# Optimization experiments

Measured on AMD Instinct MI355X. Metric: run time of the kernel, lower is better.

The kernel has to match this reference:

```python
import jax, jax.numpy as jnp
import numpy as np

HIDDEN = 4096       # in_features of gate/up proj
INTER = 11008       # intermediate_size (per projection)
GROUP = 128         # GPTQ group size
B, S = 4, 2048
NIB = jnp.uint32(0xF)


def _pack_rows(nib):
    """Pack 4-bit values along rows: [8*R, C] uint32 -> [R, C] uint32."""
    r = nib.reshape(-1, 8, nib.shape[-1])
    shifts = (jnp.arange(8, dtype=jnp.uint32) * 4)[None, :, None]
    return jnp.sum(r << shifts, axis=1, dtype=jnp.uint32)  # disjoint bits -> sum == OR


def _pack_cols(nib):
    """Pack 4-bit values along cols: [G, 8*C] uint32 -> [G, C] uint32."""
    r = nib.reshape(nib.shape[0], -1, 8)
    shifts = (jnp.arange(8, dtype=jnp.uint32) * 4)[None, None, :]
    return jnp.sum(r << shifts, axis=2, dtype=jnp.uint32)


def setup_inputs() -> dict:
    key = jax.random.key(0)
    ks = jax.random.split(key, 7)
    n_groups = HIDDEN // GROUP          # 32 groups for gate_up
    n_groups_d = INTER // GROUP         # 86 groups for down

    x = jax.random.normal(ks[0], (B, S, HIDDEN), jnp.float32)

    # gate_up_proj: in=HIDDEN, out=2*INTER
    nib_w_gu = jax.random.randint(ks[1], (HIDDEN, 2 * INTER), 0, 16).astype(jnp.uint32)
    nib_z_gu = jax.random.randint(ks[2], (n_groups, 2 * INTER), 0, 15).astype(jnp.uint32)
    qweight_gu = _pack_rows(nib_w_gu)                          # [HIDDEN//8, 2*INTER]
    qzeros_gu = _pack_cols(nib_z_gu)                           # [n_groups, 2*INTER//8]
    scales_gu = jax.random.uniform(ks[3], (n_groups, 2 * INTER), jnp.float32, 0.005, 0.02)
    g_idx_gu = (jnp.arange(HIDDEN, dtype=jnp.int32) // GROUP)

    # down_proj: in=INTER, out=HIDDEN
    nib_w_d = jax.random.randint(ks[4], (INTER, HIDDEN), 0, 16).astype(jnp.uint32)
    nib_z_d = jax.random.randint(ks[5], (n_groups_d, HIDDEN), 0, 15).astype(jnp.uint32)
    qweight_down = _pack_rows(nib_w_d)                         # [INTER//8, HIDDEN]
    qzeros_down = _pack_cols(nib_z_d)                          # [n_groups_d, HIDDEN//8]
    scales_down = jax.random.uniform(ks[6], (n_groups_d, HIDDEN), jnp.float32, 0.005, 0.02)
    g_idx_down = (jnp.arange(INTER, dtype=jnp.int32) // GROUP)

    return {
        "x": x,
        "qweight_gu": qweight_gu, "qzeros_gu": qzeros_gu,
        "scales_gu": scales_gu, "g_idx_gu": g_idx_gu,
        "qweight_down": qweight_down, "qzeros_down": qzeros_down,
        "scales_down": scales_down, "g_idx_down": g_idx_down,
    }


def _dequant(qw, qz, sc, g_idx):
    """GPTQ v2 dequant: W[i,j] = sc[g[i],j] * (wq[i,j] - (zq[g[i],j] + 1))."""
    shifts = jnp.arange(8, dtype=jnp.uint32) * 4
    # unpack qweight along rows: [R, C] -> [8*R, C]
    wq = ((qw[:, None, :] >> shifts[None, :, None]) & NIB)
    wq = wq.reshape(-1, qw.shape[1]).astype(jnp.float32)
    # unpack qzeros along cols: [G, C//8] -> [G, C]; +1 per GPTQ v2 convention
    zq = ((qz[:, :, None] >> shifts[None, None, :]) & NIB)
    zq = zq.reshape(qz.shape[0], -1).astype(jnp.float32) + 1.0
    return sc[g_idx] * (wq - zq[g_idx])  # [in, out]


def reference(x, qweight_gu, qzeros_gu, scales_gu, g_idx_gu,
              qweight_down, qzeros_down, scales_down, g_idx_down):
    w_gu = _dequant(qweight_gu, qzeros_gu, scales_gu, g_idx_gu)          # [HIDDEN, 2*INTER]
    inter = jnp.einsum('bsh,hf->bsf', x, w_gu)                            # [B,S,2*INTER]
    gate, up = inter[..., :INTER], inter[..., INTER:]
    h = jax.nn.silu(gate) * up                                            # SwiGLU
    w_d = _dequant(qweight_down, qzeros_down, scales_down, g_idx_down)   # [INTER, HIDDEN]
    return jnp.einsum('bsf,fh->bsh', h, w_d)
```

## Files before the change

### kernel.cpp

```cpp
#include <hip/hip_runtime.h>
#include <stdint.h>

#define HIDDEN 4096
#define INTER  11008
#define NTOK   8192
#define WROW   22016

typedef __bf16 bf16;
typedef __bf16 bf16x8 __attribute__((ext_vector_type(8)));
typedef _Float16 f16;
typedef _Float16 f16x2 __attribute__((ext_vector_type(2)));
typedef _Float16 f16x8 __attribute__((ext_vector_type(8)));
typedef float  f32x4  __attribute__((ext_vector_type(4)));

__device__ __forceinline__ void gload16(const void* g, void* l) {
  __builtin_amdgcn_global_load_lds(
      (const __attribute__((address_space(1))) void*)g,
      (__attribute__((address_space(3))) void*)l, 16, 0, 0);
}
__device__ __forceinline__ void gload4(const void* g, void* l) {
  __builtin_amdgcn_global_load_lds(
      (const __attribute__((address_space(1))) void*)g,
      (__attribute__((address_space(3))) void*)l, 4, 0, 0);
}

__global__ __launch_bounds__(256) void cvt_f16_kernel(const float* __restrict__ x,
                                                      f16* __restrict__ y) {
  const int i = (blockIdx.x * 256 + threadIdx.x) * 8;
  f32x4 a = *(const f32x4*)(x + i);
  f32x4 b = *(const f32x4*)(x + i + 4);
  f16x8 v;
#pragma unroll
  for (int j = 0; j < 4; ++j) { v[2 * j] = (f16)a[j]; v[2 * j + 1] = (f16)b[j]; }
  *(f16x8*)(y + i) = v;
}

__global__ __launch_bounds__(256) void spak_kernel(const uint32_t* __restrict__ qz,
                                                   const float* __restrict__ sc,
                                                   uint32_t* __restrict__ outp) {
  const int idx = blockIdx.x * 256 + threadIdx.x;
  const int gq = idx / WROW;
  const int n = idx - gq * WROW;
  const int grp = n >> 5, win = n & 31;
  const int jg = (win < 16) ? grp * 16 + win : INTER + grp * 16 + (win - 16);
  const float s = sc[(size_t)gq * WROW + jg];
  const uint32_t z = (qz[(size_t)gq * (WROW / 8) + (jg >> 3)] >> ((jg & 7) * 4)) & 15u;
  union { f16 h[2]; uint32_t u; } a, b;
  a.h[0] = (f16)s; a.h[1] = (f16)s;
  b.h[0] = (f16)(float)(1025u + z); b.h[1] = b.h[0];
  outp[(size_t)idx * 2 + 0] = a.u;
  outp[(size_t)idx * 2 + 1] = b.u;
}

__global__ __launch_bounds__(256) void dequant_kernel(const uint32_t* __restrict__ qw,
                                                      const uint32_t* __restrict__ qz,
                                                      const float* __restrict__ sc,
                                                      bf16* __restrict__ out,
                                                      int J, int Kout) {
  __shared__ __align__(16) bf16 T[64 * 256];
  const int tid = threadIdx.x;
  const int tx = tid & 63, ty = tid >> 6;
  const int j0 = blockIdx.x * 64, r0 = blockIdx.y * 32;
  const int j = j0 + tx;
  const int J8 = J >> 3;
#pragma unroll
  for (int i = 0; i < 8; ++i) {
    const int r = r0 + ty * 8 + i;
    const int g = r >> 4;
    const uint32_t w = qw[(size_t)r * J + j];
    const float s = sc[(size_t)g * J + j];
    const uint32_t zb = (qz[(size_t)g * J8 + (j >> 3)] >> ((j & 7) * 4)) & 15u;
    const float zoff = (float)(zb + 1u);
    bf16x8 v;
#pragma unroll
    for (int e = 0; e < 8; ++e) {
      const float wv = (float)((w >> (e * 4)) & 15u);
      v[e] = (bf16)(s * (wv - zoff));
    }
    const int lb = (tx * 512 + (ty * 8 + i) * 16) ^ ((tx & 31) << 4);
    *(bf16x8*)((char*)T + lb) = v;
  }
  __syncthreads();
#pragma unroll
  for (int u = 0; u < 8; ++u) {
    const int unit = u * 256 + tid;
    const int jj = unit >> 5;
    const int ob = (unit & 31) * 16;
    const int lb = (jj * 512 + ob) ^ ((jj & 31) << 4);
    bf16x8 v = *(const bf16x8*)((const char*)T + lb);
    *(bf16x8*)(out + (size_t)(j0 + jj) * Kout + r0 * 8 + (ob >> 1)) = v;
  }
}

#define OFF_BP 65536
#define OFF_SPK 82176

#define BAR __builtin_amdgcn_s_barrier()
#define LGKM0                                              \
  do {                                                     \
    asm volatile("s_waitcnt lgkmcnt(0)" ::: "memory");     \
    __builtin_amdgcn_sched_barrier(0);                     \
  } while (0)
#define VM2 asm volatile("s_waitcnt vmcnt(2)" ::: "memory")
#define VM3 asm volatile("s_waitcnt vmcnt(3)" ::: "memory")

#define STG_A(buf, h, tt)                                                      \
  do {                                                                         \
    gload16(sA00 + ((size_t)((h) * 128) * (HIDDEN * 2)) + (size_t)(tt) * 128,  \
            lds + (buf) * 32768 + (h) * 16384 + w * 1024);                     \
    gload16(sA00 + ((size_t)((h) * 128 + 64) * (HIDDEN * 2)) + (size_t)(tt) * 128, \
            lds + (buf) * 32768 + (h) * 16384 + 8192 + w * 1024);              \
  } while (0)

#define STG_B(buf, tt)                                                        \
  gload16(bsrc + (size_t)(8 * (tt) + w) * WROW,                               \
          lds + OFF_BP + (buf) * 8320 + w * 1040)

#define STG_SPK(gt)                                                           \
  gload4(spakg + ((size_t)(gt) * WROW + n0) * 2 + tid,                        \
         lds + OFF_SPK + ((gt) & 3) * 2048 + w * 256)

__device__ __forceinline__ f16x8 unpack8s(uint32_t u, f16x2 s2, f16x2 k2) {
  const uint32_t MSK = 0x000F000Fu, M = 0x64006400u;
  uint32_t q0 = (u & MSK) | M;
  uint32_t q1 = ((u >> 4) & MSK) | M;
  uint32_t q2 = ((u >> 8) & MSK) | M;
  uint32_t q3 = ((u >> 12) & MSK) | M;
  f16x2 w0 = (__builtin_bit_cast(f16x2, q0) - k2) * s2;
  f16x2 w1 = (__builtin_bit_cast(f16x2, q1) - k2) * s2;
  f16x2 w2 = (__builtin_bit_cast(f16x2, q2) - k2) * s2;
  f16x2 w3 = (__builtin_bit_cast(f16x2, q3) - k2) * s2;
  f16x8 r;
  r[0] = w0[0]; r[1] = w0[1]; r[2] = w1[0]; r[3] = w1[1];
  r[4] = w2[0]; r[5] = w2[1]; r[6] = w3[0]; r[7] = w3[1];
  return r;
}

#define UNP_SL(AVH, BUIDX, NH, NJ, KK, R, C)                                   \
  do {                                                                         \
    bv[NJ][KK] = unpack8s(bu[BUIDX], s2r[NH][NJ], k2r[NH][NJ]);                \
    _Pragma("unroll") for (int mi = 0; mi < 4; ++mi)                           \
      acc[(R) + mi][C] = __builtin_amdgcn_mfma_f32_16x16x32_f16(               \
          AVH[mi][KK], bv[NJ][KK], acc[(R) + mi][C], 0, 0, 0);                 \
  } while (0)

#define MFMA16(AVH, R, CBASE)                                                  \
  do {                                                                         \
    _Pragma("unroll") for (int kk = 0; kk < 2; ++kk)                           \
      _Pragma("unroll") for (int nj = 0; nj < 2; ++nj)                         \
        _Pragma("unroll") for (int mi = 0; mi < 4; ++mi)                       \
          acc[(R) + mi][(CBASE) + nj] = __builtin_amdgcn_mfma_f32_16x16x32_f16(\
              AVH[mi][kk], bv[nj][kk], acc[(R) + mi][(CBASE) + nj], 0, 0, 0);  \
  } while (0)

__global__ __launch_bounds__(512, 2) void gemm1q(const f16* __restrict__ A,
                                                 const uint32_t* __restrict__ qw,
                                                 const uint32_t* __restrict__ spakg,
                                                 bf16* __restrict__ H) {
  extern __shared__ char lds[];
  const int tid = threadIdx.x;
  const int lane = tid & 63, w = tid >> 6;
  const int wr = w >> 2, wc = w & 3;
  const int fr = lane & 15, fg = lane >> 4;
  constexpr int NT = HIDDEN / 64;

  const int wg = blockIdx.x;
  const int nb = wg % (WROW / 256), mb = wg / (WROW / 256);
  const int m0 = mb << 8, n0 = nb << 8;

  const int rbase = tid >> 3;
  const int cbyte0 = (tid & 7) * 16;
  const int cL0 = cbyte0 ^ ((rbase & 7) << 4);
  const char* sA00 = (const char*)A + (size_t)(m0 + rbase) * (size_t)(HIDDEN * 2) + cL0;

  const int n4 = n0 + lane * 4;
  const int grp4 = n4 >> 5, win4 = n4 & 31;
  const int jg4 = (win4 < 16) ? grp4 * 16 + win4 : INTER + grp4 * 16 + (win4 - 16);
  const uint32_t* bsrc = qw + jg4;

  const int swz = (fr & 7) << 4;
  const int ck[2] = {(fg * 16) ^ swz, (64 + fg * 16) ^ swz};
  const int aro = (wr * 64 + fr) * 128;
  auto lda = [&](int buf, int mh, int mi, int kk) -> f16x8 {
    return *(const f16x8*)(lds + buf * 32768 + mh * 16384 + aro + mi * 2048 + ck[kk]);
  };
  const int ncol[2][2] = {{wc * 32 + fr, wc * 32 + 16 + fr},
                          {wc * 32 + 128 + fr, wc * 32 + 144 + fr}};

  f32x4 acc[8][4];
#pragma unroll
  for (int i = 0; i < 8; ++i)
#pragma unroll
    for (int j = 0; j < 4; ++j) acc[i][j] = (f32x4)0.0f;
  f16x8 av0[4][2], av1[4][2], bv[2][2];
  uint32_t bu[8];
  f16x2 s2r[2][2], k2r[2][2];

  STG_SPK(0);
  STG_A(0, 0, 0);
  STG_B(0, 0);
  STG_A(0, 1, 0);
  VM2;
  BAR;

  for (int t = 0; t < NT; ++t) {
    const int cb = t & 1, nx = cb ^ 1, g = t >> 1;
    const int t1 = (t + 1 < NT) ? t + 1 : 0;

#pragma unroll
    for (int mi = 0; mi < 4; ++mi) { av0[mi][0] = lda(cb, 0, mi, 0); av0[mi][1] = lda(cb, 0, mi, 1); }
#pragma unroll
    for (int nh = 0; nh < 2; ++nh)
#pragma unroll
      for (int nj = 0; nj < 2; ++nj)
#pragma unroll
        for (int kk = 0; kk < 2; ++kk)
          bu[nh * 4 + nj * 2 + kk] = *(const uint32_t*)(
              lds + OFF_BP + cb * 8320 + (kk * 4 + fg) * 1040 + ncol[nh][nj] * 4);
    if ((t & 1) == 0) {
      const char* sp = lds + OFF_SPK + (g & 3) * 2048;
#pragma unroll
      for (int nh = 0; nh < 2; ++nh)
#pragma unroll
        for (int nj = 0; nj < 2; ++nj) {
          s2r[nh][nj] = *(const f16x2*)(sp + ncol[nh][nj] * 8);
          k2r[nh][nj] = *(const f16x2*)(sp + ncol[nh][nj] * 8 + 4);
        }
    }
    STG_A(nx, 0, t1);
    STG_B(nx, t1);
    VM3;
    BAR; LGKM0;
    __builtin_amdgcn_s_setprio(1);
    UNP_SL(av0, 0, 0, 0, 0, 0, 0);
    UNP_SL(av0, 1, 0, 0, 1, 0, 0);
    UNP_SL(av0, 2, 0, 1, 0, 0, 1);
    UNP_SL(av0, 3, 0, 1, 1, 0, 1);
    __builtin_amdgcn_s_setprio(0);
    __builtin_amdgcn_sched_barrier(0);
    BAR;

#pragma unroll
    for (int mi = 0; mi < 4; ++mi) { av1[mi][0] = lda(cb, 1, mi, 0); av1[mi][1] = lda(cb, 1, mi, 1); }
    if (t & 1) {
      const int gt = (g + 1 < 32) ? g + 1 : 31;
      STG_SPK(gt);
    }
    STG_A(nx, 1, t1);
    BAR; LGKM0;
    __builtin_amdgcn_s_setprio(1);
    MFMA16(av1, 4, 0);
    __builtin_amdgcn_s_setprio(0);
    __builtin_amdgcn_sched_barrier(0);
    BAR;

    __builtin_amdgcn_s_setprio(1);
    UNP_SL(av1, 4, 1, 0, 0, 4, 2);
    UNP_SL(av1, 5, 1, 0, 1, 4, 2);
    UNP_SL(av1, 6, 1, 1, 0, 4, 3);
    UNP_SL(av1, 7, 1, 1, 1, 4, 3);
    MFMA16(av0, 0, 2);
    __builtin_amdgcn_s_setprio(0);
    __builtin_amdgcn_sched_barrier(0);
    VM2;
    BAR;
  }
  asm volatile("s_waitcnt vmcnt(0)" ::: "memory");

#pragma unroll
  for (int mh = 0; mh < 2; ++mh)
#pragma unroll
    for (int mi = 0; mi < 4; ++mi)
#pragma unroll
      for (int nh = 0; nh < 2; ++nh) {
        const f32x4 gv4 = acc[mh * 4 + mi][nh * 2];
        const f32x4 uv4 = acc[mh * 4 + mi][nh * 2 + 1];
        const int col = (n0 >> 1) + wc * 16 + nh * 64 + fr;
#pragma unroll
        for (int rr = 0; rr < 4; ++rr) {
          const int row = m0 + wr * 64 + mh * 128 + mi * 16 + fg * 4 + rr;
          const float gv = gv4[rr], uv = uv4[rr];
          H[(size_t)row * INTER + col] = (bf16)(gv / (1.0f + __expf(-gv)) * uv);
        }
      }
}

#define OFF_A2 0
#define OFF_B2 32768

#define STG2(mat, buf, h, t)                                                   \
  do {                                                                         \
    gload16(s##mat[h][0] + (size_t)(t) * 128,                                  \
            lds + (buf) * 65536 + OFF_##mat + (h) * 16384 + w * 1024);         \
    gload16(s##mat[h][1] + (size_t)(t) * 128,                                  \
            lds + (buf) * 65536 + OFF_##mat + (h) * 16384 + 8192 + w * 1024);  \
  } while (0)
#define VM6 asm volatile("s_waitcnt vmcnt(6)" ::: "memory")

#define MFMA_Q2(MH, NH)                                                        \
  do {                                                                         \
    __builtin_amdgcn_s_setprio(1);                                             \
    _Pragma("unroll") for (int kk = 0; kk < 2; ++kk) {                         \
      _Pragma("unroll") for (int nj = 0; nj < 2; ++nj) {                       \
        _Pragma("unroll") for (int mi = 0; mi < 4; ++mi) {                     \
          acc[(MH)*4 + mi][(NH)*2 + nj] = __builtin_amdgcn_mfma_f32_16x16x32_bf16( \
              av[mi][kk], bv[nj][kk], acc[(MH)*4 + mi][(NH)*2 + nj], 0, 0, 0); \
        }                                                                      \
      }                                                                        \
    }                                                                          \
    __builtin_amdgcn_s_setprio(0);                                             \
    __builtin_amdgcn_sched_barrier(0);                                         \
  } while (0)

template <int K, int NT, int NNB>
__global__ __launch_bounds__(512, 2) void gemm8p(const bf16* __restrict__ A,
                                                 const bf16* __restrict__ Bm,
                                                 float* __restrict__ O) {
  extern __shared__ char lds[];
  const int tid = threadIdx.x;
  const int lane = tid & 63, w = tid >> 6;
  const int wr = w >> 2, wc = w & 3;
  const int fr = lane & 15, fg = lane >> 4;

  const int wg = blockIdx.x;
  const int nb = wg % NNB, mb = wg / NNB;
  const int m0 = mb << 8, n0 = nb << 8;

  const char* sA2[2][2];
  const char* sB2[2][2];
#pragma unroll
  for (int h = 0; h < 2; ++h)
#pragma unroll
    for (int l = 0; l < 2; ++l) {
      const int d = h * 16384 + (l * 512 + tid) * 16;
      const int r = d >> 7;
      const int cL = (d & 127) ^ ((r & 7) << 4);
      sA2[h][l] = (const char*)A + (size_t)(m0 + r) * (size_t)(K * 2) + cL;
      sB2[h][l] = (const char*)Bm + (size_t)(n0 + r) * (size_t)(K * 2) + cL;
    }

  const int swz = (fr & 7) << 4;
  const int ck[2] = {(fg * 16) ^ swz, (64 + fg * 16) ^ swz};
  const int aro = (wr * 64 + fr) * 128;
  const int bro = OFF_B2 + (wc * 32 + fr) * 128;

  auto lda = [&](int buf, int mh, int mi, int kk) -> bf16x8 {
    return *(const bf16x8*)(lds + buf * 65536 + mh * 16384 + aro + mi * 2048 + ck[kk]);
  };
  auto ldb = [&](int buf, int nh, int nj, int kk) -> bf16x8 {
    return *(const bf16x8*)(lds + buf * 65536 + bro + nh * 16384 + nj * 2048 + ck[kk]);
  };

  f32x4 acc[8][4];
#pragma unroll
  for (int i = 0; i < 8; ++i)
#pragma unroll
    for (int j = 0; j < 4; ++j) acc[i][j] = (f32x4)0.0f;
  bf16x8 av[4][2], bv[2][2];

  STG2(A2, 0, 0, 0);
  STG2(B2, 0, 0, 0);
  STG2(B2, 0, 1, 0);
  STG2(A2, 0, 1, 0);
  STG2(A2, 1, 0, 1);
  STG2(B2, 1, 1, 1);
  STG2(A2, 1, 1, 1);
  VM6;
  BAR;

  for (int t = 0; t < NT; ++t) {
    const int cb = t & 1, nx = cb ^ 1;
    const int t1 = (t + 1 < NT) ? t + 1 : 0;
    const int t2 = (t + 2 < NT) ? t + 2 : 0;

#pragma unroll
    for (int mi = 0; mi < 4; ++mi) { av[mi][0] = lda(cb, 0, mi, 0); av[mi][1] = lda(cb, 0, mi, 1); }
#pragma unroll
    for (int nj = 0; nj < 2; ++nj) { bv[nj][0] = ldb(cb, 0, nj, 0); bv[nj][1] = ldb(cb, 0, nj, 1); }
    STG2(B2, nx, 0, t1);
    BAR; LGKM0;
    MFMA_Q2(0, 0);
    BAR;

#pragma unroll
    for (int nj = 0; nj < 2; ++nj) { bv[nj][0] = ldb(cb, 1, nj, 0); bv[nj][1] = ldb(cb, 1, nj, 1); }
    STG2(A2, cb, 0, t2);
    BAR; LGKM0;
    MFMA_Q2(0, 1);
    BAR;

#pragma unroll
    for (int mi = 0; mi < 4; ++mi) { av[mi][0] = lda(cb, 1, mi, 0); av[mi][1] = lda(cb, 1, mi, 1); }
    STG2(B2, cb, 1, t2);
    BAR; LGKM0;
    MFMA_Q2(1, 1);
    BAR;

#pragma unroll
    for (int nj = 0; nj < 2; ++nj) { bv[nj][0] = ldb(cb, 0, nj, 0); bv[nj][1] = ldb(cb, 0, nj, 1); }
    STG2(A2, cb, 1, t2);
    VM6;
    BAR; LGKM0;
    MFMA_Q2(1, 0);
    BAR;
  }

#pragma unroll
  for (int mh = 0; mh < 2; ++mh)
#pragma unroll
    for (int mi = 0; mi < 4; ++mi)
#pragma unroll
      for (int nh = 0; nh < 2; ++nh)
#pragma unroll
        for (int nj = 0; nj < 2; ++nj) {
          const f32x4 a = acc[mh * 4 + mi][nh * 2 + nj];
          const int col = n0 + wc * 32 + nh * 128 + nj * 16 + fr;
#pragma unroll
          for (int rr = 0; rr < 4; ++rr) {
            const int row = m0 + wr * 64 + mh * 128 + mi * 16 + fg * 4 + rr;
            __builtin_nontemporal_store(a[rr], &O[(size_t)row * HIDDEN + col]);
          }
        }
}

extern "C" void kernel_launch(void* const* d_in, const int* in_sizes, int n_in,
                              void* d_out, int out_size, void* d_ws, size_t ws_size,
                              hipStream_t stream) {
  (void)in_sizes; (void)n_in; (void)out_size; (void)ws_size;
  const float*    x     = (const float*)d_in[0];
  const uint32_t* qw_gu = (const uint32_t*)d_in[1];
  const uint32_t* qz_gu = (const uint32_t*)d_in[2];
  const float*    sc_gu = (const float*)d_in[3];
  const uint32_t* qw_d  = (const uint32_t*)d_in[5];
  const uint32_t* qz_d  = (const uint32_t*)d_in[6];
  const float*    sc_d  = (const float*)d_in[7];
  float*          out   = (float*)d_out;

  char* ws = (char*)d_ws;
  const size_t XB  = (size_t)NTOK * HIDDEN * 2;
  const size_t W2B = (size_t)HIDDEN * INTER * 2;
  const size_t HB  = (size_t)NTOK * INTER * 2;
  f16*      xb    = (f16*)ws;
  bf16*     wt    = (bf16*)(ws + XB);
  bf16*     hb    = (bf16*)(ws + XB + W2B);
  uint32_t* spakg = (uint32_t*)(ws + XB + W2B + HB);

  hipFuncSetAttribute((const void*)&gemm1q,
                      hipFuncAttributeMaxDynamicSharedMemorySize, 90368);
  hipFuncSetAttribute((const void*)&gemm8p<INTER, INTER / 64, HIDDEN / 256>,
                      hipFuncAttributeMaxDynamicSharedMemorySize, 131072);

  cvt_f16_kernel<<<NTOK * HIDDEN / 2048, 256, 0, stream>>>(x, xb);
  spak_kernel<<<32 * WROW / 256, 256, 0, stream>>>(qz_gu, sc_gu, spakg);

  gemm1q<<<(WROW / 256) * (NTOK / 256), 512, 90368, stream>>>(xb, qw_gu, spakg, hb);

  dequant_kernel<<<dim3(HIDDEN / 64, (INTER / 8) / 32), 256, 0, stream>>>(
      qw_d, qz_d, sc_d, wt, HIDDEN, INTER);
  gemm8p<INTER, INTER / 64, HIDDEN / 256>
      <<<(HIDDEN / 256) * (NTOK / 256), 512, 131072, stream>>>(hb, wt, out);
}
```

Baseline: 2.125 ms.

## Pre-permute gate/up packed weights into per-tile layout for vectorized LDS reads

Adds a repack kernel that permutes the packed gate/up weights into a per-block, per-k-tile layout matching the MFMA fragment order. The GEMM then stages B with a contiguous 16-byte load per thread and reads the eight packed words per lane as two 128-bit LDS loads, replacing eight scalar LDS reads from a padded layout. The B stage buffer loses its padding. This costs an extra pass over the gate/up weights each call and more workspace, and the new LDS layout may raise bank conflicts.

```diff
diff --git a/kernel.cpp b/kernel.cpp
--- a/kernel.cpp
+++ b/kernel.cpp
@@ -12,6 +12,7 @@
 typedef _Float16 f16x2 __attribute__((ext_vector_type(2)));
 typedef _Float16 f16x8 __attribute__((ext_vector_type(8)));
 typedef float  f32x4  __attribute__((ext_vector_type(4)));
+typedef unsigned int u32x4 __attribute__((ext_vector_type(4)));
 
 __device__ __forceinline__ void gload16(const void* g, void* l) {
   __builtin_amdgcn_global_load_lds(
@@ -52,6 +53,24 @@
   outp[(size_t)idx * 2 + 1] = b.u;
 }
 
+__global__ __launch_bounds__(256) void repackB_kernel(const uint32_t* __restrict__ qw,
+                                                      uint32_t* __restrict__ outp) {
+  const size_t idx = (size_t)blockIdx.x * 256 + threadIdx.x;
+  const int c = (int)(idx & 2047);
+  const int kt = (int)((idx >> 11) & 63);
+  const int nb = (int)(idx >> 17);
+  const int j = c & 3;
+  const int chunk = c >> 2;
+  const int r = chunk >> 6;
+  const int wc = (chunk >> 4) & 3;
+  const int fr = chunk & 15;
+  const int col = wc * 32 + fr + (j & 1) * 16 + (j >> 1) * 128;
+  const int n = nb * 256 + col;
+  const int grp = n >> 5, win = n & 31;
+  const int jg = (win < 16) ? grp * 16 + win : INTER + grp * 16 + (win - 16);
+  outp[idx] = qw[(size_t)(kt * 8 + r) * WROW + jg];
+}
+
 __global__ __launch_bounds__(256) void dequant_kernel(const uint32_t* __restrict__ qw,
                                                       const uint32_t* __restrict__ qz,
                                                       const float* __restrict__ sc,
@@ -93,7 +112,7 @@
 }
 
 #define OFF_BP 65536
-#define OFF_SPK 82176
+#define OFF_SPK 81920
 
 #define BAR __builtin_amdgcn_s_barrier()
 #define LGKM0                                              \
@@ -112,9 +131,9 @@
             lds + (buf) * 32768 + (h) * 16384 + 8192 + w * 1024);              \
   } while (0)
 
-#define STG_B(buf, tt)                                                        \
-  gload16(bsrc + (size_t)(8 * (tt) + w) * WROW,                               \
-          lds + OFF_BP + (buf) * 8320 + w * 1040)
+#define STG_B(buf, tt)                                                         \
+  gload16(repk_src + (size_t)(tt) * 2048 + tid * 4,                            \
+          lds + OFF_BP + (buf) * 8192 + tid * 16)
 
 #define STG_SPK(gt)                                                           \
   gload4(spakg + ((size_t)(gt) * WROW + n0) * 2 + tid,                        \
@@ -154,7 +173,7 @@
   } while (0)
 
 __global__ __launch_bounds__(512, 2) void gemm1q(const f16* __restrict__ A,
-                                                 const uint32_t* __restrict__ qw,
+                                                 const uint32_t* __restrict__ repk,
                                                  const uint32_t* __restrict__ spakg,
                                                  bf16* __restrict__ H) {
   extern __shared__ char lds[];
@@ -173,10 +192,7 @@
   const int cL0 = cbyte0 ^ ((rbase & 7) << 4);
   const char* sA00 = (const char*)A + (size_t)(m0 + rbase) * (size_t)(HIDDEN * 2) + cL0;
 
-  const int n4 = n0 + lane * 4;
-  const int grp4 = n4 >> 5, win4 = n4 & 31;
-  const int jg4 = (win4 < 16) ? grp4 * 16 + win4 : INTER + grp4 * 16 + (win4 - 16);
-  const uint32_t* bsrc = qw + jg4;
+  const uint32_t* repk_src = repk + (size_t)nb * 64 * 2048;
 
   const int swz = (fr & 7) << 4;
   const int ck[2] = {(fg * 16) ^ swz, (64 + fg * 16) ^ swz};
@@ -184,6 +200,7 @@
   auto lda = [&](int buf, int mh, int mi, int kk) -> f16x8 {
     return *(const f16x8*)(lds + buf * 32768 + mh * 16384 + aro + mi * 2048 + ck[kk]);
   };
+  const int c1b = ((fg * 4 + wc) * 16 + fr) * 16;
   const int ncol[2][2] = {{wc * 32 + fr, wc * 32 + 16 + fr},
                           {wc * 32 + 128 + fr, wc * 32 + 144 + fr}};
 
@@ -209,14 +226,12 @@
 
 #pragma unroll
     for (int mi = 0; mi < 4; ++mi) { av0[mi][0] = lda(cb, 0, mi, 0); av0[mi][1] = lda(cb, 0, mi, 1); }
-#pragma unroll
-    for (int nh = 0; nh < 2; ++nh)
-#pragma unroll
-      for (int nj = 0; nj < 2; ++nj)
-#pragma unroll
-        for (int kk = 0; kk < 2; ++kk)
-          bu[nh * 4 + nj * 2 + kk] = *(const uint32_t*)(
-              lds + OFF_BP + cb * 8320 + (kk * 4 + fg) * 1040 + ncol[nh][nj] * 4);
+    {
+      u32x4 v1 = *(const u32x4*)(lds + OFF_BP + cb * 8192 + c1b);
+      u32x4 v2 = *(const u32x4*)(lds + OFF_BP + cb * 8192 + c1b + 4096);
+      bu[0] = v1.x; bu[1] = v2.x; bu[2] = v1.y; bu[3] = v2.y;
+      bu[4] = v1.z; bu[5] = v2.z; bu[6] = v1.w; bu[7] = v2.w;
+    }
     if ((t & 1) == 0) {
       const char* sp = lds + OFF_SPK + (g & 3) * 2048;
 #pragma unroll
@@ -440,20 +455,23 @@
   const size_t XB  = (size_t)NTOK * HIDDEN * 2;
   const size_t W2B = (size_t)HIDDEN * INTER * 2;
   const size_t HB  = (size_t)NTOK * INTER * 2;
+  const size_t SPB = (size_t)32 * WROW * 2 * 4;
   f16*      xb    = (f16*)ws;
   bf16*     wt    = (bf16*)(ws + XB);
   bf16*     hb    = (bf16*)(ws + XB + W2B);
   uint32_t* spakg = (uint32_t*)(ws + XB + W2B + HB);
+  uint32_t* repk  = (uint32_t*)(ws + XB + W2B + HB + SPB);
 
   hipFuncSetAttribute((const void*)&gemm1q,
-                      hipFuncAttributeMaxDynamicSharedMemorySize, 90368);
+                      hipFuncAttributeMaxDynamicSharedMemorySize, 90112);
   hipFuncSetAttribute((const void*)&gemm8p<INTER, INTER / 64, HIDDEN / 256>,
                       hipFuncAttributeMaxDynamicSharedMemorySize, 131072);
 
   cvt_f16_kernel<<<NTOK * HIDDEN / 2048, 256, 0, stream>>>(x, xb);
   spak_kernel<<<32 * WROW / 256, 256, 0, stream>>>(qz_gu, sc_gu, spakg);
-
-  gemm1q<<<(WROW / 256) * (NTOK / 256), 512, 90368, stream>>>(xb, qw_gu, spakg, hb);
+  repackB_kernel<<<((WROW / 256) * 64 * 2048) / 256, 256, 0, stream>>>(qw_gu, repk);
+
+  gemm1q<<<(WROW / 256) * (NTOK / 256), 512, 90112, stream>>>(xb, repk, spakg, hb);
 
   dequant_kernel<<<dim3(HIDDEN / 64, (INTER / 8) / 32), 256, 0, stream>>>(
       qw_d, qz_d, sc_d, wt, HIDDEN, INTER);
```

After: 2.113 ms. About the same (-0.6%).
